# Kernel tuning notes

Measured on AMD Instinct MI355X. Metric: run time of the kernel, lower is better.

The kernel has to match this reference:

```python
import jax, jax.numpy as jnp
import numpy as np

H = 128   # hidden_size
E = 100   # embedding/input_size
V = 1000  # vocabulary_size
FD = 512  # feature_extractor_dim
N, TQ, TA = 512, 64, 64


def _cell(x, h, c, Wih, Whh, b):
    # PyTorch LSTM cell, gate order i,f,g,o; b = b_ih + b_hh fused.
    z = x @ Wih.T + h @ Whh.T + b
    i, f, g, o = jnp.split(z, 4, axis=-1)
    c = jax.nn.sigmoid(f) * c + jax.nn.sigmoid(i) * jnp.tanh(g)
    h = jax.nn.sigmoid(o) * jnp.tanh(c)
    return h, c


def setup_inputs() -> dict:
    key = jax.random.key(0)
    ks = iter(jax.random.split(key, 40))
    def w(shape, s=0.08):
        return (s * jax.random.normal(next(ks), shape)).astype(jnp.float32)
    inp = {
        "questions": jax.random.randint(next(ks), (N, TQ), 0, V),
        "answers": jax.random.randint(next(ks), (N, TA), 0, V),
        "answer_lens": jax.random.randint(next(ks), (N,), 1, TA + 1),
        "img": w((FD,), 1.0),  # pre-extracted image features (feature_extractor = identity)
        "emb": w((V, E), 0.1),
    }
    for p in ("enc", "dec"):
        inp[p + "_Wih0"] = w((4 * H, E)); inp[p + "_Whh0"] = w((4 * H, H)); inp[p + "_b0"] = w((4 * H,))
        inp[p + "_Wih1"] = w((4 * H, H)); inp[p + "_Whh1"] = w((4 * H, H)); inp[p + "_b1"] = w((4 * H,))
    inp["Wk"] = w((H, H)); inp["bk"] = w((H,))
    inp["Wout"] = w((V, 3 * H + FD)); inp["bout"] = w((V,))
    return inp


def reference(questions, answers, answer_lens, img, emb,
              enc_Wih0, enc_Whh0, enc_b0, enc_Wih1, enc_Whh1, enc_b1,
              dec_Wih0, dec_Whh0, dec_b0, dec_Wih1, dec_Whh1, dec_b1,
              Wk, bk, Wout, bout):
    n, tq = questions.shape
    # ---- encode: 2-layer LSTM over all questions (batched), keys projection ----
    qe = emb[questions]                               # [N,TQ,E]
    z = jnp.zeros((n, H), emb.dtype)
    def enc_step(carry, x_t):
        h0, c0, h1, c1 = carry
        h0, c0 = _cell(x_t, h0, c0, enc_Wih0, enc_Whh0, enc_b0)
        h1, c1 = _cell(h0, h1, c1, enc_Wih1, enc_Whh1, enc_b1)
        return (h0, c0, h1, c1), h1
    (eh0, ec0, eh1, ec1), outs = jax.lax.scan(enc_step, (z, z, z, z), qe.swapaxes(0, 1))
    keys = outs.swapaxes(0, 1) @ Wk.T + bk            # [N,TQ,H]; decode uses keys as values too

    # ---- decode: sequential over questions (history carry), scan over timesteps ----
    ae = emb[answers]                                  # [N,TA,E]
    mask = (jnp.arange(answers.shape[1])[None, :] < answer_lens[:, None]).astype(emb.dtype)

    def q_step(history, xs):
        emb_q, k_q, h0, c0, h1, c1, m_q = xs
        def t_step(carry, x_t):
            h0, c0, h1, c1 = carry
            h0, c0 = _cell(x_t, h0, c0, dec_Wih0, dec_Whh0, dec_b0)
            h1, c1 = _cell(h0, h1, c1, dec_Wih1, dec_Whh1, dec_b1)
            ctx = jax.nn.softmax(k_q @ h1) @ k_q       # dot-product attention, v := k (as in source)
            feat = jnp.concatenate([h1, ctx, history, img], axis=-1)  # [3H+FD]
            return (h0, c0, h1, c1), feat @ Wout.T + bout
        carry, logits = jax.lax.scan(t_step, (h0, c0, h1, c1), emb_q)
        return carry[2], logits * m_q[:, None]         # history <- last-layer h; mask ragged tail

    _, logits = jax.lax.scan(q_step, jnp.zeros((H,), emb.dtype),
                             (ae, keys, eh0, ec0, eh1, ec1, mask))
    return logits                                      # [N,TA,V], zero-padded past answer_lens
```

## Files before the change

kernel.cpp:

```cpp
#include <hip/hip_runtime.h>
#include <stdint.h>

#define HD   128
#define ED   100
#define VD   1000
#define FDV  512
#define NS   512
#define TT   64
#define MT   (NS*TT)

typedef __attribute__((ext_vector_type(8))) short  short8;
typedef __attribute__((ext_vector_type(4))) float  f32x4;

__device__ __forceinline__ float blo(uint32_t u){ return __uint_as_float(u << 16); }
__device__ __forceinline__ float bhi(uint32_t u){ return __uint_as_float(u & 0xffff0000u); }
__device__ __forceinline__ uint16_t f2bf(float f){
  uint32_t x = __float_as_uint(f);
  return (uint16_t)((x + 0x7fffu + ((x >> 16) & 1u)) >> 16);
}
__device__ __forceinline__ float sigf(float x){ return 1.f/(1.f+__expf(-x)); }
__device__ __forceinline__ float ftanh(float x){
  float ax = fabsf(x);
  float e = __expf(-2.f*ax);
  float t = (1.f - e) / (1.f + e);
  return copysignf(t, x);
}

struct ConvJob { const float* s; uint16_t* d; int R, C, Cp; };
struct ConvJobs { ConvJob j[11]; };

__global__ void k_convert(ConvJobs jobs){
  int stride = gridDim.x * blockDim.x;
  int tid0 = blockIdx.x * blockDim.x + threadIdx.x;
  for (int ji = 0; ji < 11; ++ji){
    const ConvJob jb = jobs.j[ji];
    int total = jb.R * jb.Cp;
    for (int i = tid0; i < total; i += stride){
      int r = i / jb.Cp, c = i - r*jb.Cp;
      float v = (c < jb.C) ? jb.s[(size_t)r*jb.C + c] : 0.f;
      jb.d[i] = f2bf(v);
    }
  }
}

__global__ void k_gather(const uint16_t* __restrict__ embP, const int* __restrict__ tok,
                         uint16_t* __restrict__ out){
  int i = blockIdx.x * blockDim.x + threadIdx.x;
  if (i >= MT*16) return;
  int m = i >> 4, c8 = i & 15;
  int v = tok[m];
  ((uint4*)(out + (size_t)m*128))[c8] = ((const uint4*)(embP + (size_t)v*128))[c8];
}

template<int MODE>
__global__ __launch_bounds__(256) void k_gemm(
    const uint16_t* __restrict__ A, const uint16_t* __restrict__ W,
    const float* __restrict__ bias, void* __restrict__ out,
    int N, int K, const int* __restrict__ lens)
{
  __shared__ __align__(16) uint16_t lsA[128][40];
  __shared__ __align__(16) uint16_t lsB[128][40];
  const int tid = threadIdx.x;
  const int m0 = blockIdx.x * 128, n0 = blockIdx.y * 128;
  const int l = tid & 63, w = tid >> 6;
  const int wm = (w >> 1) * 64, wn = (w & 1) * 64;
  const int fr = l & 15, fo = (l >> 4) * 8;
  f32x4 acc[4][4] = {};
  for (int kt = 0; kt < K; kt += 32) {
    #pragma unroll
    for (int u = 0; u < 2; ++u) {
      int c = tid + u * 256;
      int row = c >> 2, ko = (c & 3) << 3;
      uint4 av = *(const uint4*)(A + (size_t)(m0 + row) * K + kt + ko);
      *(uint4*)(&lsA[row][ko]) = av;
      int nr = n0 + row;
      uint4 bv = make_uint4(0u,0u,0u,0u);
      if (nr < N) bv = *(const uint4*)(W + (size_t)nr * K + kt + ko);
      *(uint4*)(&lsB[row][ko]) = bv;
    }
    __syncthreads();
    short8 af[4], bfv[4];
    #pragma unroll
    for (int i = 0; i < 4; ++i) af[i]  = *(const short8*)(&lsA[wm + i*16 + fr][fo]);
    #pragma unroll
    for (int j = 0; j < 4; ++j) bfv[j] = *(const short8*)(&lsB[wn + j*16 + fr][fo]);
    #pragma unroll
    for (int i = 0; i < 4; ++i)
      #pragma unroll
      for (int j = 0; j < 4; ++j)
        acc[i][j] = __builtin_amdgcn_mfma_f32_16x16x32_bf16(af[i], bfv[j], acc[i][j], 0, 0, 0);
    __syncthreads();
  }
  const int r0 = (l >> 4) * 4, cc = l & 15;
  #pragma unroll
  for (int j = 0; j < 4; ++j) {
    int col = n0 + wn + j*16 + cc;
    if (col >= N) continue;
    float bv = bias[col];
    #pragma unroll
    for (int i = 0; i < 4; ++i) {
      #pragma unroll
      for (int r = 0; r < 4; ++r) {
        int row = m0 + wm + i*16 + r0 + r;
        float v = acc[i][j][r] + bv;
        if (MODE == 1) {
          ((uint16_t*)out)[(size_t)row * N + col] = f2bf(v);
        } else if (MODE == 2) {
          int t = row & 63, n = row >> 6;
          if (t >= lens[n]) v = 0.f;
          ((float*)out)[(size_t)row * N + col] = v;
        } else {
          ((float*)out)[(size_t)row * N + col] = v;
        }
      }
    }
  }
}

__global__ __launch_bounds__(512) void k_lstm_mfma(
    const uint16_t* __restrict__ X,
    const uint16_t* __restrict__ Whh,
    const float* __restrict__ h0i, const float* __restrict__ c0i,
    uint16_t* __restrict__ hout,
    float* __restrict__ hfin, float* __restrict__ cfin)
{
  __shared__ __align__(16) uint16_t hbuf[2][16][136];
  const int n0 = blockIdx.x * 16;
  const int w = threadIdx.x >> 6, l = threadIdx.x & 63;
  const int s = l & 15;
  const int hi4 = l >> 4;
  const int j0 = w*16 + hi4*4;

  short8 afr[4][4];
  #pragma unroll
  for (int g = 0; g < 4; ++g)
    #pragma unroll
    for (int kk = 0; kk < 4; ++kk)
      afr[g][kk] = *(const short8*)(Whh + (size_t)(g*128 + w*16 + s)*128 + kk*32 + hi4*8);

  f32x4 cst = {0.f, 0.f, 0.f, 0.f};
  if (c0i) cst = *(const f32x4*)(c0i + (size_t)(n0+s)*128 + j0);
  {
    uint16_t hb[4] = {0,0,0,0};
    if (h0i) {
      float4 hv = *(const float4*)(h0i + (size_t)(n0+s)*128 + j0);
      hb[0]=f2bf(hv.x); hb[1]=f2bf(hv.y); hb[2]=f2bf(hv.z); hb[3]=f2bf(hv.w);
    }
    *(uint2*)(&hbuf[0][s][j0]) = *(const uint2*)hb;
  }
  __syncthreads();

  const uint16_t* Xp = X + (size_t)(n0+s)*TT*512 + j0;
  uint2 xv[4], xvn[4];
  #pragma unroll
  for (int g = 0; g < 4; ++g) xv[g] = *(const uint2*)(Xp + g*128);

  float hfv[4] = {0.f,0.f,0.f,0.f};
  for (int t = 0; t < TT; ++t) {
    const int rb = t & 1;
    if (t + 1 < TT) {
      const uint16_t* Xn = Xp + (size_t)(t+1)*512;
      #pragma unroll
      for (int g = 0; g < 4; ++g) xvn[g] = *(const uint2*)(Xn + g*128);
    }
    short8 bfr[4];
    #pragma unroll
    for (int kk = 0; kk < 4; ++kk)
      bfr[kk] = *(const short8*)(&hbuf[rb][s][kk*32 + hi4*8]);
    f32x4 acc[4] = {{0.f,0.f,0.f,0.f},{0.f,0.f,0.f,0.f},{0.f,0.f,0.f,0.f},{0.f,0.f,0.f,0.f}};
    #pragma unroll
    for (int kk = 0; kk < 4; ++kk)
      #pragma unroll
      for (int g = 0; g < 4; ++g)
        acc[g] = __builtin_amdgcn_mfma_f32_16x16x32_bf16(afr[g][kk], bfr[kk], acc[g], 0, 0, 0);
    uint16_t hb[4];
    #pragma unroll
    for (int r = 0; r < 4; ++r) {
      uint32_t wi = (r & 2) ? xv[0].y : xv[0].x;
      uint32_t wf = (r & 2) ? xv[1].y : xv[1].x;
      uint32_t wg = (r & 2) ? xv[2].y : xv[2].x;
      uint32_t wo = (r & 2) ? xv[3].y : xv[3].x;
      float zi = acc[0][r] + ((r & 1) ? bhi(wi) : blo(wi));
      float zf = acc[1][r] + ((r & 1) ? bhi(wf) : blo(wf));
      float zg = acc[2][r] + ((r & 1) ? bhi(wg) : blo(wg));
      float zo = acc[3][r] + ((r & 1) ? bhi(wo) : blo(wo));
      float cn = sigf(zf) * cst[r] + sigf(zi) * ftanh(zg);
      float h  = sigf(zo) * ftanh(cn);
      cst[r] = cn;
      hfv[r] = h;
      hb[r] = f2bf(h);
    }
    *(uint2*)(&hbuf[rb ^ 1][s][j0]) = *(const uint2*)hb;
    *(uint2*)(hout + ((size_t)(n0+s)*TT + t)*HD + j0) = *(const uint2*)hb;
    if (t + 1 < TT) {
      #pragma unroll
      for (int g = 0; g < 4; ++g) xv[g] = xvn[g];
    }
    __syncthreads();
  }
  if (hfin) *(float4*)(hfin + (size_t)(n0+s)*128 + j0) = make_float4(hfv[0],hfv[1],hfv[2],hfv[3]);
  if (cfin) *(float4*)(cfin + (size_t)(n0+s)*128 + j0) = make_float4(cst[0],cst[1],cst[2],cst[3]);
}

__global__ __launch_bounds__(256) void k_attn(
    const float* __restrict__ keys,
    const uint16_t* __restrict__ h1,
    uint16_t* __restrict__ feat)
{
  __shared__ float ks[64][129];
  __shared__ float ps[4][64];
  const int n = blockIdx.x;
  for (int i = threadIdx.x; i < 64*128; i += 256)
    ks[i >> 7][i & 127] = keys[(size_t)n*8192 + i];
  __syncthreads();
  const int w = threadIdx.x >> 6, l = threadIdx.x & 63;
  for (int tt = 0; tt < 16; ++tt) {
    const int t = tt*4 + w;
    const int m = n*64 + t;
    const uint4* hp = (const uint4*)(h1 + (size_t)m*128);
    float s = 0.f;
    #pragma unroll
    for (int k = 0; k < 16; ++k) {
      uint4 hv = hp[k];
      s += ks[l][8*k+0]*blo(hv.x) + ks[l][8*k+1]*bhi(hv.x)
         + ks[l][8*k+2]*blo(hv.y) + ks[l][8*k+3]*bhi(hv.y)
         + ks[l][8*k+4]*blo(hv.z) + ks[l][8*k+5]*bhi(hv.z)
         + ks[l][8*k+6]*blo(hv.w) + ks[l][8*k+7]*bhi(hv.w);
    }
    float mx = s;
    #pragma unroll
    for (int o = 32; o; o >>= 1) mx = fmaxf(mx, __shfl_xor(mx, o));
    float p = __expf(s - mx);
    float sm = p;
    #pragma unroll
    for (int o = 32; o; o >>= 1) sm += __shfl_xor(sm, o);
    p /= sm;
    ps[w][l] = p;
    float c0 = 0.f, c1 = 0.f;
    #pragma unroll
    for (int q = 0; q < 64; ++q) {
      float pq = ps[w][q];
      c0 += pq * ks[q][l];
      c1 += pq * ks[q][l + 64];
    }
    feat[(size_t)m*896 + 128 + l] = f2bf(c0);
    feat[(size_t)m*896 + 192 + l] = f2bf(c1);
  }
}

__global__ void k_feat(const uint16_t* __restrict__ h1, const float* __restrict__ img,
                       uint16_t* __restrict__ feat){
  int i = blockIdx.x * blockDim.x + threadIdx.x;
  if (i >= MT*96) return;
  int m = i / 96, c8 = i - m*96;
  int c = c8 * 8;
  if (c < 128) {
    uint4 v = ((const uint4*)(h1 + (size_t)m*128))[c8];
    *(uint4*)(feat + (size_t)m*896 + c) = v;
  } else if (c < 256) {
    int n = m >> 6;
    uint4 v = make_uint4(0u,0u,0u,0u);
    if (n > 0) v = ((const uint4*)(h1 + ((size_t)(n-1)*64 + 63)*128))[c8 - 16];
    *(uint4*)(feat + (size_t)m*896 + 128 + c) = v;
  } else {
    const float4* ip = (const float4*)img;
    float4 f0 = ip[(c - 256) >> 2], f1 = ip[((c - 256) >> 2) + 1];
    uint16_t o[8];
    o[0]=f2bf(f0.x); o[1]=f2bf(f0.y); o[2]=f2bf(f0.z); o[3]=f2bf(f0.w);
    o[4]=f2bf(f1.x); o[5]=f2bf(f1.y); o[6]=f2bf(f1.z); o[7]=f2bf(f1.w);
    *(uint4*)(feat + (size_t)m*896 + 128 + c) = *(uint4*)o;
  }
}

extern "C" void kernel_launch(void* const* d_in, const int* in_sizes, int n_in,
                              void* d_out, int out_size, void* d_ws, size_t ws_size,
                              hipStream_t stream) {
  const int*   questions = (const int*)d_in[0];
  const int*   answers   = (const int*)d_in[1];
  const int*   lens      = (const int*)d_in[2];
  const float* img       = (const float*)d_in[3];
  const float* emb       = (const float*)d_in[4];
  const float* eWih0 = (const float*)d_in[5],  *eWhh0 = (const float*)d_in[6],  *eB0 = (const float*)d_in[7];
  const float* eWih1 = (const float*)d_in[8],  *eWhh1 = (const float*)d_in[9],  *eB1 = (const float*)d_in[10];
  const float* dWih0 = (const float*)d_in[11], *dWhh0 = (const float*)d_in[12], *dB0 = (const float*)d_in[13];
  const float* dWih1 = (const float*)d_in[14], *dWhh1 = (const float*)d_in[15], *dB1 = (const float*)d_in[16];
  const float* Wk   = (const float*)d_in[17], *bk   = (const float*)d_in[18];
  const float* Wout = (const float*)d_in[19], *bout = (const float*)d_in[20];

  char* ws = (char*)d_ws;
  size_t off = 0;
  auto alloc = [&](size_t n)->char* {
    char* p = ws + off; off += (n + 255) & ~(size_t)255; return p;
  };
  uint16_t* embP  = (uint16_t*)alloc((size_t)VD*128*2);
  uint16_t* wih0e = (uint16_t*)alloc(512*128*2);
  uint16_t* whh0e = (uint16_t*)alloc(512*128*2);
  uint16_t* wih1e = (uint16_t*)alloc(512*128*2);
  uint16_t* whh1e = (uint16_t*)alloc(512*128*2);
  uint16_t* wih0d = (uint16_t*)alloc(512*128*2);
  uint16_t* whh0d = (uint16_t*)alloc(512*128*2);
  uint16_t* wih1d = (uint16_t*)alloc(512*128*2);
  uint16_t* whh1d = (uint16_t*)alloc(512*128*2);
  uint16_t* wkb   = (uint16_t*)alloc(128*128*2);
  uint16_t* woutb = (uint16_t*)alloc((size_t)VD*896*2);
  uint16_t* embBuf= (uint16_t*)alloc((size_t)MT*128*2);
  uint16_t* Xbuf  = (uint16_t*)alloc((size_t)MT*512*2);
  uint16_t* hA    = (uint16_t*)alloc((size_t)MT*128*2);
  uint16_t* h1b   = (uint16_t*)alloc((size_t)MT*128*2);
  float*    keysf = (float*)   alloc((size_t)MT*128*4);
  uint16_t* feat  = (uint16_t*)alloc((size_t)MT*896*2);
  float* eh0 = (float*)alloc(NS*128*4);
  float* ec0 = (float*)alloc(NS*128*4);
  float* eh1 = (float*)alloc(NS*128*4);
  float* ec1 = (float*)alloc(NS*128*4);
  if (off > ws_size) return;

  ConvJobs jobs;
  jobs.j[0]  = {emb,   embP,  VD, ED, 128};
  jobs.j[1]  = {eWih0, wih0e, 512, ED, 128};
  jobs.j[2]  = {eWhh0, whh0e, 512, 128, 128};
  jobs.j[3]  = {eWih1, wih1e, 512, 128, 128};
  jobs.j[4]  = {eWhh1, whh1e, 512, 128, 128};
  jobs.j[5]  = {dWih0, wih0d, 512, ED, 128};
  jobs.j[6]  = {dWhh0, whh0d, 512, 128, 128};
  jobs.j[7]  = {dWih1, wih1d, 512, 128, 128};
  jobs.j[8]  = {dWhh1, whh1d, 512, 128, 128};
  jobs.j[9]  = {Wk,    wkb,   128, 128, 128};
  jobs.j[10] = {Wout,  woutb, VD, 896, 896};
  hipLaunchKernelGGL(k_convert, dim3(1024), dim3(256), 0, stream, jobs);

  hipLaunchKernelGGL(k_gather, dim3(MT*16/256), dim3(256), 0, stream, embP, questions, embBuf);
  hipLaunchKernelGGL(k_gemm<1>, dim3(MT/128, 4), dim3(256), 0, stream, embBuf, wih0e, eB0, Xbuf, 512, 128, nullptr);
  hipLaunchKernelGGL(k_lstm_mfma, dim3(NS/16), dim3(512), 0, stream, Xbuf, whh0e, (const float*)nullptr, (const float*)nullptr, hA, eh0, ec0);
  hipLaunchKernelGGL(k_gemm<1>, dim3(MT/128, 4), dim3(256), 0, stream, hA, wih1e, eB1, Xbuf, 512, 128, nullptr);
  hipLaunchKernelGGL(k_lstm_mfma, dim3(NS/16), dim3(512), 0, stream, Xbuf, whh1e, (const float*)nullptr, (const float*)nullptr, h1b, eh1, ec1);
  hipLaunchKernelGGL(k_gemm<0>, dim3(MT/128, 1), dim3(256), 0, stream, h1b, wkb, bk, keysf, 128, 128, nullptr);

  hipLaunchKernelGGL(k_gather, dim3(MT*16/256), dim3(256), 0, stream, embP, answers, embBuf);
  hipLaunchKernelGGL(k_gemm<1>, dim3(MT/128, 4), dim3(256), 0, stream, embBuf, wih0d, dB0, Xbuf, 512, 128, nullptr);
  hipLaunchKernelGGL(k_lstm_mfma, dim3(NS/16), dim3(512), 0, stream, Xbuf, whh0d, eh0, ec0, hA, (float*)nullptr, (float*)nullptr);
  hipLaunchKernelGGL(k_gemm<1>, dim3(MT/128, 4), dim3(256), 0, stream, hA, wih1d, dB1, Xbuf, 512, 128, nullptr);
  hipLaunchKernelGGL(k_lstm_mfma, dim3(NS/16), dim3(512), 0, stream, Xbuf, whh1d, eh1, ec1, h1b, (float*)nullptr, (float*)nullptr);

  hipLaunchKernelGGL(k_attn, dim3(NS), dim3(256), 0, stream, keysf, h1b, feat);
  hipLaunchKernelGGL(k_feat, dim3((MT*96+255)/256), dim3(256), 0, stream, h1b, img, feat);
  hipLaunchKernelGGL(k_gemm<2>, dim3(MT/128, 8), dim3(256), 0, stream, feat, woutb, bout, d_out, VD, 896, lens);
}
```

Baseline: 931.7 us.

## Use direct global-to-LDS loads in GEMM, fuse feature assembly into attention

The GEMM tile loads now use global_load_lds to write straight into unpadded shared memory, with no register round trip. The Wout weights are zero-padded to 1024 rows so the N-bound check can go. The grid is transposed so consecutive blocks share an A row-tile, which should improve L2 reuse. The separate feature-assembly kernel is folded into the attention kernel, with img pre-converted to bf16 once, removing one launch and a pass over feat. The risks are LDS bank conflicts from dropping the padding, and the epilogue must still guard columns beyond 1000.

```diff
diff --git a/kernel.cpp b/kernel.cpp
--- a/kernel.cpp
+++ b/kernel.cpp
@@ -12,6 +12,9 @@
 typedef __attribute__((ext_vector_type(8))) short  short8;
 typedef __attribute__((ext_vector_type(4))) float  f32x4;
 
+typedef const __attribute__((address_space(1))) uint16_t* gas_u16;
+typedef __attribute__((address_space(3))) uint16_t*       las_u16;
+
 __device__ __forceinline__ float blo(uint32_t u){ return __uint_as_float(u << 16); }
 __device__ __forceinline__ float bhi(uint32_t u){ return __uint_as_float(u & 0xffff0000u); }
 __device__ __forceinline__ uint16_t f2bf(float f){
@@ -26,18 +29,18 @@
   return copysignf(t, x);
 }
 
-struct ConvJob { const float* s; uint16_t* d; int R, C, Cp; };
-struct ConvJobs { ConvJob j[11]; };
+struct ConvJob { const float* s; uint16_t* d; int R, R0, C, Cp; };
+struct ConvJobs { ConvJob j[12]; };
 
 __global__ void k_convert(ConvJobs jobs){
   int stride = gridDim.x * blockDim.x;
   int tid0 = blockIdx.x * blockDim.x + threadIdx.x;
-  for (int ji = 0; ji < 11; ++ji){
+  for (int ji = 0; ji < 12; ++ji){
     const ConvJob jb = jobs.j[ji];
     int total = jb.R * jb.Cp;
     for (int i = tid0; i < total; i += stride){
       int r = i / jb.Cp, c = i - r*jb.Cp;
-      float v = (c < jb.C) ? jb.s[(size_t)r*jb.C + c] : 0.f;
+      float v = (r < jb.R0 && c < jb.C) ? jb.s[(size_t)r*jb.C + c] : 0.f;
       jb.d[i] = f2bf(v);
     }
   }
@@ -58,25 +61,27 @@
     const float* __restrict__ bias, void* __restrict__ out,
     int N, int K, const int* __restrict__ lens)
 {
-  __shared__ __align__(16) uint16_t lsA[128][40];
-  __shared__ __align__(16) uint16_t lsB[128][40];
+  __shared__ __align__(16) uint16_t lsA[128][32];
+  __shared__ __align__(16) uint16_t lsB[128][32];
   const int tid = threadIdx.x;
-  const int m0 = blockIdx.x * 128, n0 = blockIdx.y * 128;
+  const int n0 = blockIdx.x * 128, m0 = blockIdx.y * 128;
   const int l = tid & 63, w = tid >> 6;
   const int wm = (w >> 1) * 64, wn = (w & 1) * 64;
   const int fr = l & 15, fo = (l >> 4) * 8;
+  const int srow = w*16 + (l >> 2);
+  const int sce  = (l & 3) * 8;
   f32x4 acc[4][4] = {};
   for (int kt = 0; kt < K; kt += 32) {
     #pragma unroll
     for (int u = 0; u < 2; ++u) {
-      int c = tid + u * 256;
-      int row = c >> 2, ko = (c & 3) << 3;
-      uint4 av = *(const uint4*)(A + (size_t)(m0 + row) * K + kt + ko);
-      *(uint4*)(&lsA[row][ko]) = av;
-      int nr = n0 + row;
-      uint4 bv = make_uint4(0u,0u,0u,0u);
-      if (nr < N) bv = *(const uint4*)(W + (size_t)nr * K + kt + ko);
-      *(uint4*)(&lsB[row][ko]) = bv;
+      const int row = u*64 + srow;
+      const int lo  = w*512 + u*2048;
+      __builtin_amdgcn_global_load_lds(
+          (gas_u16)(A + (size_t)(m0 + row) * K + kt + sce),
+          (las_u16)(&lsA[0][0] + lo), 16, 0, 0);
+      __builtin_amdgcn_global_load_lds(
+          (gas_u16)(W + (size_t)(n0 + row) * K + kt + sce),
+          (las_u16)(&lsB[0][0] + lo), 16, 0, 0);
     }
     __syncthreads();
     short8 af[4], bfv[4];
@@ -205,6 +210,7 @@
 __global__ __launch_bounds__(256) void k_attn(
     const float* __restrict__ keys,
     const uint16_t* __restrict__ h1,
+    const uint16_t* __restrict__ imgb,
     uint16_t* __restrict__ feat)
 {
   __shared__ float ks[64][129];
@@ -212,12 +218,15 @@
   const int n = blockIdx.x;
   for (int i = threadIdx.x; i < 64*128; i += 256)
     ks[i >> 7][i & 127] = keys[(size_t)n*8192 + i];
+  const int w = threadIdx.x >> 6, l = threadIdx.x & 63;
+  uint32_t hd = 0;
+  if (n > 0) hd = ((const uint32_t*)(h1 + ((size_t)(n-1)*64 + 63)*128))[l];
+  const uint4 iv = ((const uint4*)imgb)[l];
   __syncthreads();
-  const int w = threadIdx.x >> 6, l = threadIdx.x & 63;
   for (int tt = 0; tt < 16; ++tt) {
     const int t = tt*4 + w;
-    const int m = n*64 + t;
-    const uint4* hp = (const uint4*)(h1 + (size_t)m*128);
+    const size_t m = (size_t)n*64 + t;
+    const uint4* hp = (const uint4*)(h1 + m*128);
     float s = 0.f;
     #pragma unroll
     for (int k = 0; k < 16; ++k) {
@@ -243,32 +252,12 @@
       c0 += pq * ks[q][l];
       c1 += pq * ks[q][l + 64];
     }
-    feat[(size_t)m*896 + 128 + l] = f2bf(c0);
-    feat[(size_t)m*896 + 192 + l] = f2bf(c1);
-  }
-}
-
-__global__ void k_feat(const uint16_t* __restrict__ h1, const float* __restrict__ img,
-                       uint16_t* __restrict__ feat){
-  int i = blockIdx.x * blockDim.x + threadIdx.x;
-  if (i >= MT*96) return;
-  int m = i / 96, c8 = i - m*96;
-  int c = c8 * 8;
-  if (c < 128) {
-    uint4 v = ((const uint4*)(h1 + (size_t)m*128))[c8];
-    *(uint4*)(feat + (size_t)m*896 + c) = v;
-  } else if (c < 256) {
-    int n = m >> 6;
-    uint4 v = make_uint4(0u,0u,0u,0u);
-    if (n > 0) v = ((const uint4*)(h1 + ((size_t)(n-1)*64 + 63)*128))[c8 - 16];
-    *(uint4*)(feat + (size_t)m*896 + 128 + c) = v;
-  } else {
-    const float4* ip = (const float4*)img;
-    float4 f0 = ip[(c - 256) >> 2], f1 = ip[((c - 256) >> 2) + 1];
-    uint16_t o[8];
-    o[0]=f2bf(f0.x); o[1]=f2bf(f0.y); o[2]=f2bf(f0.z); o[3]=f2bf(f0.w);
-    o[4]=f2bf(f1.x); o[5]=f2bf(f1.y); o[6]=f2bf(f1.z); o[7]=f2bf(f1.w);
-    *(uint4*)(feat + (size_t)m*896 + 128 + c) = *(uint4*)o;
+    uint16_t* fr_ = feat + m*896;
+    ((uint32_t*)fr_)[l] = ((const uint32_t*)(h1 + m*128))[l];
+    fr_[128 + l] = f2bf(c0);
+    fr_[192 + l] = f2bf(c1);
+    ((uint32_t*)(fr_ + 256))[l] = hd;
+    ((uint4*)(fr_ + 384))[l] = iv;
   }
 }
 
@@ -302,7 +291,8 @@
   uint16_t* wih1d = (uint16_t*)alloc(512*128*2);
   uint16_t* whh1d = (uint16_t*)alloc(512*128*2);
   uint16_t* wkb   = (uint16_t*)alloc(128*128*2);
-  uint16_t* woutb = (uint16_t*)alloc((size_t)VD*896*2);
+  uint16_t* woutb = (uint16_t*)alloc((size_t)1024*896*2);
+  uint16_t* imgb  = (uint16_t*)alloc(512*2);
   uint16_t* embBuf= (uint16_t*)alloc((size_t)MT*128*2);
   uint16_t* Xbuf  = (uint16_t*)alloc((size_t)MT*512*2);
   uint16_t* hA    = (uint16_t*)alloc((size_t)MT*128*2);
@@ -316,33 +306,33 @@
   if (off > ws_size) return;
 
   ConvJobs jobs;
-  jobs.j[0]  = {emb,   embP,  VD, ED, 128};
-  jobs.j[1]  = {eWih0, wih0e, 512, ED, 128};
-  jobs.j[2]  = {eWhh0, whh0e, 512, 128, 128};
-  jobs.j[3]  = {eWih1, wih1e, 512, 128, 128};
-  jobs.j[4]  = {eWhh1, whh1e, 512, 128, 128};
-  jobs.j[5]  = {dWih0, wih0d, 512, ED, 128};
-  jobs.j[6]  = {dWhh0, whh0d, 512, 128, 128};
-  jobs.j[7]  = {dWih1, wih1d, 512, 128, 128};
-  jobs.j[8]  = {dWhh1, whh1d, 512, 128, 128};
-  jobs.j[9]  = {Wk,    wkb,   128, 128, 128};
-  jobs.j[10] = {Wout,  woutb, VD, 896, 896};
+  jobs.j[0]  = {emb,   embP,  VD,  VD,  ED,  128};
+  jobs.j[1]  = {eWih0, wih0e, 512, 512, ED,  128};
+  jobs.j[2]  = {eWhh0, whh0e, 512, 512, 128, 128};
+  jobs.j[3]  = {eWih1, wih1e, 512, 512, 128, 128};
+  jobs.j[4]  = {eWhh1, whh1e, 512, 512, 128, 128};
+  jobs.j[5]  = {dWih0, wih0d, 512, 512, ED,  128};
+  jobs.j[6]  = {dWhh0, whh0d, 512, 512, 128, 128};
+  jobs.j[7]  = {dWih1, wih1d, 512, 512, 128, 128};
+  jobs.j[8]  = {dWhh1, whh1d, 512, 512, 128, 128};
+  jobs.j[9]  = {Wk,    wkb,   128, 128, 128, 128};
+  jobs.j[10] = {Wout,  woutb, 1024, VD, 896, 896};
+  jobs.j[11] = {img,   imgb,  1,   1,   512, 512};
   hipLaunchKernelGGL(k_convert, dim3(1024), dim3(256), 0, stream, jobs);
 
   hipLaunchKernelGGL(k_gather, dim3(MT*16/256), dim3(256), 0, stream, embP, questions, embBuf);
-  hipLaunchKernelGGL(k_gemm<1>, dim3(MT/128, 4), dim3(256), 0, stream, embBuf, wih0e, eB0, Xbuf, 512, 128, nullptr);
+  hipLaunchKernelGGL(k_gemm<1>, dim3(4, MT/128), dim3(256), 0, stream, embBuf, wih0e, eB0, Xbuf, 512, 128, nullptr);
   hipLaunchKernelGGL(k_lstm_mfma, dim3(NS/16), dim3(512), 0, stream, Xbuf, whh0e, (const float*)nullptr, (const float*)nullptr, hA, eh0, ec0);
-  hipLaunchKernelGGL(k_gemm<1>, dim3(MT/128, 4), dim3(256), 0, stream, hA, wih1e, eB1, Xbuf, 512, 128, nullptr);
+  hipLaunchKernelGGL(k_gemm<1>, dim3(4, MT/128), dim3(256), 0, stream, hA, wih1e, eB1, Xbuf, 512, 128, nullptr);
   hipLaunchKernelGGL(k_lstm_mfma, dim3(NS/16), dim3(512), 0, stream, Xbuf, whh1e, (const float*)nullptr, (const float*)nullptr, h1b, eh1, ec1);
-  hipLaunchKernelGGL(k_gemm<0>, dim3(MT/128, 1), dim3(256), 0, stream, h1b, wkb, bk, keysf, 128, 128, nullptr);
+  hipLaunchKernelGGL(k_gemm<0>, dim3(1, MT/128), dim3(256), 0, stream, h1b, wkb, bk, keysf, 128, 128, nullptr);
 
   hipLaunchKernelGGL(k_gather, dim3(MT*16/256), dim3(256), 0, stream, embP, answers, embBuf);
-  hipLaunchKernelGGL(k_gemm<1>, dim3(MT/128, 4), dim3(256), 0, stream, embBuf, wih0d, dB0, Xbuf, 512, 128, nullptr);
+  hipLaunchKernelGGL(k_gemm<1>, dim3(4, MT/128), dim3(256), 0, stream, embBuf, wih0d, dB0, Xbuf, 512, 128, nullptr);
   hipLaunchKernelGGL(k_lstm_mfma, dim3(NS/16), dim3(512), 0, stream, Xbuf, whh0d, eh0, ec0, hA, (float*)nullptr, (float*)nullptr);
-  hipLaunchKernelGGL(k_gemm<1>, dim3(MT/128, 4), dim3(256), 0, stream, hA, wih1d, dB1, Xbuf, 512, 128, nullptr);
+  hipLaunchKernelGGL(k_gemm<1>, dim3(4, MT/128), dim3(256), 0, stream, hA, wih1d, dB1, Xbuf, 512, 128, nullptr);
   hipLaunchKernelGGL(k_lstm_mfma, dim3(NS/16), dim3(512), 0, stream, Xbuf, whh1d, eh1, ec1, h1b, (float*)nullptr, (float*)nullptr);
 
-  hipLaunchKernelGGL(k_attn, dim3(NS), dim3(256), 0, stream, keysf, h1b, feat);
-  hipLaunchKernelGGL(k_feat, dim3((MT*96+255)/256), dim3(256), 0, stream, h1b, img, feat);
-  hipLaunchKernelGGL(k_gemm<2>, dim3(MT/128, 8), dim3(256), 0, stream, feat, woutb, bout, d_out, VD, 896, lens);
-}
+  hipLaunchKernelGGL(k_attn, dim3(NS), dim3(256), 0, stream, keysf, h1b, imgb, feat);
+  hipLaunchKernelGGL(k_gemm<2>, dim3(8, MT/128), dim3(256), 0, stream, feat, woutb, bout, d_out, VD, 896, lens);
+}
```

Result: faster. 901.5 us (-3.2%).
